# Kernel optimization log

Measured on AMD Instinct MI355X. Metric: run time of the kernel, lower is better.

## Reference

```python
import jax, jax.numpy as jnp
import numpy as np

EPS = 1e-3  # mesh.epsilon boundary margin
N_GRID = 96
F_DIM = 512


def setup_inputs() -> dict:
    key = jax.random.key(0)
    n = N_GRID
    idx = np.arange(n * n).reshape(n, n)
    # triangulated grid mesh: horizontal, vertical and diagonal edges
    e_h = np.stack([idx[:, :-1].ravel(), idx[:, 1:].ravel()])
    e_v = np.stack([idx[:-1, :].ravel(), idx[1:, :].ravel()])
    e_d = np.stack([idx[:-1, :-1].ravel(), idx[1:, 1:].ravel()])
    edges = np.concatenate([e_h, e_v, e_d], axis=1).astype(np.int32)  # [2, E]
    ys, xs = np.meshgrid(np.linspace(0.0, 1.0, n), np.linspace(0.0, 1.0, n), indexing="ij")
    vs = np.stack([xs.ravel(), ys.ravel()], axis=1).astype(np.float32)  # [V, 2]
    image = jax.random.normal(key, (n * n, F_DIM), dtype=jnp.float32)  # [V, F]
    return {"image": image, "edges": jnp.asarray(edges), "vs": jnp.asarray(vs)}


def _decimate(edges, order, adj0, boundary_v, out_target):
    """Sequential greedy edge collapse; returns (final vertex mask, collapsed flag per sorted slot).
    All carries are int/bool so this loop carries no gradient."""
    V = adj0.shape[0]
    E = order.shape[0]

    def cond(state):
        adj, mask, count, ptr, collapsed = state
        return (count > out_target) & (ptr < E)

    def body(state):
        adj, mask, count, ptr, collapsed = state
        eid = order[ptr]
        v0 = edges[0, eid]
        v1 = edges[1, eid]
        alive = mask[v0] & mask[v1]
        # neighbor sets (row | column of directed adjacency), as in is_valid
        n0 = adj[:, v0] | adj[v0, :]
        n1 = adj[:, v1] | adj[v1, :]
        shared2 = jnp.sum(n0 & n1) == 2
        do = alive & (~(boundary_v[v0] | boundary_v[v1])) & shared2

        def merge(op):
            adj, mask, count, collapsed = op
            adj = adj.at[v0, :].set(adj[v0, :] | adj[v1, :])
            adj = adj.at[:, v0].set(adj[:, v0] | adj[:, v1])
            adj = adj.at[v1, :].set(False)
            adj = adj.at[:, v1].set(False)
            adj = adj.at[v0, v0].set(False)
            mask = mask.at[v1].set(False)
            collapsed = collapsed.at[ptr].set(True)
            return adj, mask, count - 1, collapsed

        adj, mask, count, collapsed = jax.lax.cond(
            do, merge, lambda op: op, (adj, mask, count, collapsed))
        return adj, mask, count, ptr + 1, collapsed

    init = (adj0, jnp.ones((V,), dtype=bool), jnp.int32(V), jnp.int32(0),
            jnp.zeros((E,), dtype=bool))
    _, mask, _, _, collapsed = jax.lax.while_loop(cond, body, init)
    return mask, collapsed


def reference(image, edges, vs):
    V, F = image.shape
    e0, e1 = edges[0], edges[1]
    # priority = squared magnitude of concat(image[e0], image[e1]) per edge
    sq = jnp.sum(image * image, axis=1)  # [V]
    prio = sq[e0] + sq[e1]               # [E]
    # static heap pop order == stable ascending sort (ties broken by edge id)
    order = jnp.argsort(prio)
    adj0 = jnp.zeros((V, V), dtype=bool).at[e0, e1].set(True)
    b = ((vs[:, 0] < EPS) | (vs[:, 0] > 1.0 - EPS) |
         (vs[:, 1] < EPS) | (vs[:, 1] > 1.0 - EPS))
    mask, collapsed = _decimate(edges, order, adj0, b, V // 2)

    # replay collapses on features (merge_vertex -> average endpoint features)
    def step(feat, inp):
        eid, flag = inp
        v0 = edges[0, eid]
        v1 = edges[1, eid]
        feat = feat.at[v0].set(jnp.where(flag, 0.5 * (feat[v0] + feat[v1]), feat[v0]))
        return feat, None

    feat, _ = jax.lax.scan(step, image, (order, collapsed))
    return feat * mask[:, None].astype(feat.dtype)
```

## Files before the change

### kernel.cpp

```cpp
#include <hip/hip_runtime.h>
#include <stdint.h>

#define F_DIM 512
#define CAP   64
#define MAXV  9216
#define GP    4

typedef unsigned long long u64;

__global__ void k_sq(const float* __restrict__ img, double* __restrict__ sqd, int V) {
  int v = blockIdx.x;
  if (v >= V) return;
  const float* row = img + (size_t)v * F_DIM;
  double s = 0.0;
  for (int f = threadIdx.x; f < F_DIM; f += 64) {
    double x = (double)row[f];
    s += x * x;
  }
  for (int off = 32; off > 0; off >>= 1) s += __shfl_down(s, off);
  if (threadIdx.x == 0) sqd[v] = s;
}

__global__ void k_prep(const float* __restrict__ vs, const int* __restrict__ edges,
                       int V, int E, int* __restrict__ deg, unsigned char* __restrict__ elig) {
  int i = blockIdx.x * blockDim.x + threadIdx.x;
  if (i < V) deg[i] = 0;
  if (i < E) {
    int a = edges[i], b = edges[E + i];
    float ax = vs[2 * a], ay = vs[2 * a + 1];
    float bx = vs[2 * b], by = vs[2 * b + 1];
    const float eps = 1e-3f;
    const float hi = 1.0f - 1e-3f;
    bool ba = (ax < eps) || (ax > hi) || (ay < eps) || (ay > hi);
    bool bb = (bx < eps) || (bx > hi) || (by < eps) || (by > hi);
    elig[i] = (!ba && !bb) ? 1 : 0;
  }
}

__global__ void k_lists(const int* __restrict__ edges, int E,
                        int* __restrict__ deg, unsigned short* __restrict__ nbr) {
  int e = blockIdx.x * blockDim.x + threadIdx.x;
  if (e >= E) return;
  int a = edges[e], b = edges[E + e];
  int ia = atomicAdd(&deg[a], 1);
  nbr[a * CAP + ia] = (unsigned short)b;
  int ib = atomicAdd(&deg[b], 1);
  nbr[b * CAP + ib] = (unsigned short)a;
}

__global__ void k_keys(const double* __restrict__ sqd, const int* __restrict__ edges,
                       int E, int P, u64* __restrict__ keys) {
  int e = blockIdx.x * blockDim.x + threadIdx.x;
  if (e >= P) return;
  if (e < E) {
    double prio = sqd[edges[e]] + sqd[edges[E + e]];
    u64 bits = (u64)__double_as_longlong(prio);
    keys[e] = (bits & ~0xFFFFull) | (u64)e;
  } else {
    keys[e] = ~0ull;
  }
}

#define SCH 4096
__global__ void __launch_bounds__(1024)
k_sort(u64* __restrict__ keys, int n) {
  __shared__ u64 buf[SCH];
  int tid = threadIdx.x;
  int nt = blockDim.x;
  int ch = n < SCH ? n : SCH;
  for (int chunk = 0; chunk < n; chunk += ch) {
    for (int i = tid; i < ch; i += nt) buf[i] = keys[chunk + i];
    __syncthreads();
    for (int k = 2; k <= ch; k <<= 1) {
      for (int j = k >> 1; j > 0; j >>= 1) {
        for (int li = tid; li < ch; li += nt) {
          int lj = li ^ j;
          if (lj > li) {
            u64 x = buf[li], y = buf[lj];
            bool up = (((chunk + li) & k) == 0);
            if (up ? (x > y) : (x < y)) { buf[li] = y; buf[lj] = x; }
          }
        }
        __syncthreads();
      }
    }
    for (int i = tid; i < ch; i += nt) keys[chunk + i] = buf[i];
    __syncthreads();
  }
  for (int k = (ch << 1); k <= n; k <<= 1) {
    for (int j = k >> 1; j >= ch; j >>= 1) {
      for (int i = tid; i < n; i += nt) {
        int ixj = i ^ j;
        if (ixj > i) {
          u64 x = keys[i], y = keys[ixj];
          bool up = ((i & k) == 0);
          if (up ? (x > y) : (x < y)) { keys[i] = y; keys[ixj] = x; }
        }
      }
      __syncthreads();
    }
    for (int chunk = 0; chunk < n; chunk += ch) {
      for (int i = tid; i < ch; i += nt) buf[i] = keys[chunk + i];
      __syncthreads();
      for (int j = ch >> 1; j > 0; j >>= 1) {
        for (int li = tid; li < ch; li += nt) {
          int lj = li ^ j;
          if (lj > li) {
            u64 x = buf[li], y = buf[lj];
            bool up = (((chunk + li) & k) == 0);
            if (up ? (x > y) : (x < y)) { buf[li] = y; buf[lj] = x; }
          }
        }
        __syncthreads();
      }
      for (int i = tid; i < ch; i += nt) keys[chunk + i] = buf[i];
      __syncthreads();
    }
  }
}

__global__ void k_reorder(const u64* __restrict__ keys, const int* __restrict__ edges,
                          const unsigned char* __restrict__ elig, int E,
                          unsigned* __restrict__ packed) {
  int t = blockIdx.x * blockDim.x + threadIdx.x;
  if (t >= E) return;
  int eid = (int)(keys[t] & 0xFFFFull);
  unsigned v0 = (unsigned)edges[eid];
  unsigned v1 = (unsigned)edges[E + eid];
  unsigned el = (unsigned)elig[eid];
  packed[t] = v0 | (v1 << 14) | (el << 28);
}

__device__ __forceinline__ int findroot(unsigned* rs, int x) {
  while (true) {
    unsigned w = rs[x];
    int p = (int)(w & 0xFFFFu);
    if (p == x) return x;
    int q = (int)(rs[p] & 0xFFFFu);
    if (q == p) return p;
    rs[x] = (w & 0xFFFF0000u) | (unsigned)q;
    x = q;
  }
}

__global__ void __launch_bounds__(64, 1)
k_decimate(int E, int V, int target, const unsigned* __restrict__ packed,
           const int* __restrict__ deg_g, unsigned short* __restrict__ nbr,
           int2* __restrict__ events, int* __restrict__ nev_out) {
  __shared__ unsigned rs[MAXV];
  __shared__ unsigned short mkA0[MAXV], mkB0[MAXV];
  __shared__ unsigned short mkA1[MAXV], mkB1[MAXV];
  const int lane = threadIdx.x;
  const int lane_h = lane & 31;
  if (V > MAXV) return;
  for (int v = lane; v < V; v += 64) {
    rs[v] = (unsigned)v | ((unsigned)deg_g[v] << 16);
    mkA0[v] = 0; mkB0[v] = 0; mkA1[v] = 0; mkB1[v] = 0;
  }
  __syncthreads();

  int count = V, nev = 0;
  unsigned ctr = 0;
  bool stop = false, dirty = false;
  const u64 lanebit = 1ull << lane;
  const u64 below = lanebit - 1;

  auto bumpCtr = [&]() {
    ++ctr;
    if ((ctr & 1023u) == 0u) {
      for (int v = lane; v < MAXV; v += 64) { mkA0[v] = 0; mkB0[v] = 0; mkA1[v] = 0; mkB1[v] = 0; }
      asm volatile("s_waitcnt lgkmcnt(0)" ::: "memory");
      __builtin_amdgcn_sched_barrier(0);
      ++ctr;
    }
  };

  auto solo = [&](int cv0, int cv1) -> bool {
    unsigned w0 = rs[cv0], w1 = rs[cv1];
    if ((w0 & 0xFFFFu) != (unsigned)cv0 || (w1 & 0xFFFFu) != (unsigned)cv1) return false;
    int L0 = (int)(w0 >> 16), L1 = (int)(w1 >> 16);
    if (dirty) {
      asm volatile("s_waitcnt vmcnt(0)" ::: "memory");
      __builtin_amdgcn_sched_barrier(0);
      dirty = false;
    }
    unsigned rawA = (lane < L0) ? (unsigned)nbr[cv0 * CAP + lane] : 0u;
    unsigned rawB = (lane < L1) ? (unsigned)nbr[cv1 * CAP + lane] : 0u;
    int rA = 0x7FFF, rB = 0x7FFF;
    if (lane < L0) rA = findroot(rs, (int)rawA);
    if (lane < L1) rB = findroot(rs, (int)rawB);
    bumpCtr();
    unsigned tag = ctr & 1023u;
    unsigned short enc = (unsigned short)((tag << 6) | (unsigned)lane);
    bool wA = (lane < L0) && (rA != cv0);
    bool wB = (lane < L1) && (rB != cv1);
    if (wA) mkA0[rA] = enc;
    if (wB) mkB0[rB] = enc;
    asm volatile("s_waitcnt lgkmcnt(0)" ::: "memory");
    __builtin_amdgcn_sched_barrier(0);
    bool canonA = wA && (mkA0[rA] == enc);
    bool canonB = wB && (mkB0[rB] == enc);
    bool sh = canonA && ((mkB0[rA] >> 6) == tag);
    if (__popcll(__ballot(sh)) != 2) return false;
    if (L0 + L1 <= CAP) {
      if (lane < L1) nbr[cv0 * CAP + L0 + lane] = (unsigned short)rB;
      if (lane == 0) rs[cv0] = (unsigned)cv0 | ((unsigned)(L0 + L1) << 16);
    } else {
      bool pa = canonA && (rA != cv1);
      bool pb = canonB && (rB != cv0) && ((mkA0[rB] >> 6) != tag);
      u64 ma = __ballot(pa);
      u64 mb = __ballot(pb);
      int na = __popcll(ma);
      int tot = na + __popcll(mb);
      if (tot > CAP) tot = CAP;
      if (pa) nbr[cv0 * CAP + __popcll(ma & below)] = (unsigned short)rA;
      if (pb) {
        int pos = na + __popcll(mb & below);
        if (pos < CAP) nbr[cv0 * CAP + pos] = (unsigned short)rB;
      }
      if (lane == 0) rs[cv0] = (unsigned)cv0 | ((unsigned)tot << 16);
    }
    if (lane == 0) {
      rs[cv1] = (unsigned)cv0;
      events[nev] = make_int2(cv0, cv1);
    }
    asm volatile("s_waitcnt lgkmcnt(0)" ::: "memory");
    __builtin_amdgcn_sched_barrier(0);
    return true;
  };

  for (int base = 0; base < E && !stop; base += 64) {
    int t = base + lane;
    unsigned pk = (t < E) ? packed[t] : 0u;
    int mv0 = (int)(pk & 0x3FFFu);
    int mv1 = (int)((pk >> 14) & 0x3FFFu);
    bool cand = (t < E) && ((pk >> 28) & 1u) &&
                (rs[mv0] & 0xFFFFu) == (unsigned)mv0 &&
                (rs[mv1] & 0xFFFFu) == (unsigned)mv1;
    u64 cm = __ballot(cand);

    while (cm != 0 && !stop) {
      int c0A[GP], c1A[GP], c0B[GP], c1B[GP];
      unsigned ga[GP], gb[GP];
#pragma unroll
      for (int p = 0; p < GP; ++p) {
        int idA = -1, idB = -1;
        if (cm) { idA = __builtin_ctzll(cm); cm &= cm - 1; }
        if (cm) { idB = __builtin_ctzll(cm); cm &= cm - 1; }
        if (idA >= 0) {
          unsigned pkc = __builtin_amdgcn_readlane(pk, idA);
          c0A[p] = (int)(pkc & 0x3FFFu); c1A[p] = (int)((pkc >> 14) & 0x3FFFu);
        } else { c0A[p] = -1; c1A[p] = -1; }
        if (idB >= 0) {
          unsigned pkc = __builtin_amdgcn_readlane(pk, idB);
          c0B[p] = (int)(pkc & 0x3FFFu); c1B[p] = (int)((pkc >> 14) & 0x3FFFu);
        } else { c0B[p] = -1; c1B[p] = -1; }
      }
      if (dirty) {
        asm volatile("s_waitcnt vmcnt(0)" ::: "memory");
        __builtin_amdgcn_sched_barrier(0);
        dirty = false;
      }
#pragma unroll
      for (int p = 0; p < GP; ++p) {
        int cv0h = (lane < 32) ? c0A[p] : c0B[p];
        int cv1h = (lane < 32) ? c1A[p] : c1B[p];
        if (cv0h >= 0) {
          ga[p] = (unsigned)nbr[cv0h * CAP + lane_h];
          gb[p] = (unsigned)nbr[cv1h * CAP + lane_h];
        } else { ga[p] = 0; gb[p] = 0; }
      }
      int app[2 * GP];
#pragma unroll
      for (int j = 0; j < 2 * GP; ++j) app[j] = -1;

#pragma unroll
      for (int p = 0; p < GP; ++p) {
        if (c0A[p] < 0 || stop) continue;
        bool stale = false;
#pragma unroll
        for (int j = 0; j < 2 * GP; ++j) {
          if (j < 2 * p && app[j] >= 0) {
            stale = stale || app[j] == c0A[p] || app[j] == c1A[p] ||
                             app[j] == c0B[p] || app[j] == c1B[p];
          }
        }
        if (stale) {
          asm volatile("s_waitcnt vmcnt(0)" ::: "memory");
          __builtin_amdgcn_sched_barrier(0);
          dirty = false;
          int cv0h = (lane < 32) ? c0A[p] : c0B[p];
          int cv1h = (lane < 32) ? c1A[p] : c1B[p];
          if (cv0h >= 0) {
            ga[p] = (unsigned)nbr[cv0h * CAP + lane_h];
            gb[p] = (unsigned)nbr[cv1h * CAP + lane_h];
          }
        }
        int cv0 = (lane < 32) ? c0A[p] : c0B[p];
        int cv1 = (lane < 32) ? c1A[p] : c1B[p];
        bool halfAct = cv0 >= 0;
        unsigned w0 = 0, w1 = 0;
        if (halfAct) { w0 = rs[cv0]; w1 = rs[cv1]; }
        bool alive = halfAct && (w0 & 0xFFFFu) == (unsigned)cv0 &&
                                (w1 & 0xFFFFu) == (unsigned)cv1;
        int L0 = alive ? (int)(w0 >> 16) : 0;
        int L1 = alive ? (int)(w1 >> 16) : 0;
        bool paired = alive && L0 <= 32 && L1 <= 32;
        bool soloH = alive && !paired;
        u64 aliveBal = __ballot(alive);
        u64 soloBal = __ballot(soloH);
        bumpCtr();
        unsigned tag = ctr & 1023u;
        int rA = 0x7FFF, rB = 0x7FFF;
        if (paired && lane_h < L0) rA = findroot(rs, (int)(ga[p] & 0xFFFFu));
        if (paired && lane_h < L1) rB = findroot(rs, (int)(gb[p] & 0xFFFFu));
        unsigned short* mA = (lane < 32) ? mkA0 : mkA1;
        unsigned short* mB = (lane < 32) ? mkB0 : mkB1;
        unsigned short enc = (unsigned short)((tag << 6) | (unsigned)lane);
        bool wA = paired && lane_h < L0 && rA != cv0;
        bool wB = paired && lane_h < L1 && rB != cv1;
        if (wA) mA[rA] = enc;
        if (wB) mB[rB] = enc;
        asm volatile("s_waitcnt lgkmcnt(0)" ::: "memory");
        __builtin_amdgcn_sched_barrier(0);
        bool sh = wA && (mA[rA] == enc) && ((mB[rA] >> 6) == tag);
        u64 shBal = __ballot(sh);
        int cntA = __popcll(shBal & 0xFFFFFFFFull);
        int cntB = __popcll(shBal >> 32);
        bool aliveA = (aliveBal & 1ull) != 0;
        bool aliveB = ((aliveBal >> 32) & 1ull) != 0;
        bool soloA = (soloBal & 1ull) != 0;
        bool soloB = ((soloBal >> 32) & 1ull) != 0;
        int L0A = __builtin_amdgcn_readlane(L0, 0);
        int L1A = __builtin_amdgcn_readlane(L1, 0);
        int L0B = __builtin_amdgcn_readlane(L0, 32);
        int L1B = __builtin_amdgcn_readlane(L1, 32);
        bool committedA = false;
        if (aliveA) {
          if (soloA) {
            committedA = solo(c0A[p], c1A[p]);
          } else if (cntA == 2) {
            if (lane < 32 && lane_h < L1A)
              nbr[c0A[p] * CAP + L0A + lane_h] = (unsigned short)rB;
            if (lane == 0) {
              rs[c0A[p]] = (unsigned)c0A[p] | ((unsigned)(L0A + L1A) << 16);
              rs[c1A[p]] = (unsigned)c0A[p];
              events[nev] = make_int2(c0A[p], c1A[p]);
            }
            asm volatile("s_waitcnt lgkmcnt(0)" ::: "memory");
            __builtin_amdgcn_sched_barrier(0);
            committedA = true;
          }
          if (committedA) {
            app[2 * p] = c0A[p];
            nev++; count--; dirty = true;
            if (count <= target) stop = true;
          }
        }
        if (!stop && c0B[p] >= 0 && aliveB) {
          bool deadB = false, soloNeedB = soloB;
          if (committedA) {
            int c1a = c1A[p], c0a = c0A[p];
            if (c0B[p] == c1a || c1B[p] == c1a) deadB = true;
            else {
              u64 hb = __ballot((rA == c1a) || (rB == c1a));
              if (c0B[p] == c0a || c1B[p] == c0a || (hb >> 32) != 0ull) soloNeedB = true;
            }
          }
          if (!deadB) {
            bool commitB = false;
            if (soloNeedB) {
              commitB = solo(c0B[p], c1B[p]);
            } else if (cntB == 2) {
              if (lane >= 32 && lane_h < L1B)
                nbr[c0B[p] * CAP + L0B + lane_h] = (unsigned short)rB;
              if (lane == 0) {
                rs[c0B[p]] = (unsigned)c0B[p] | ((unsigned)(L0B + L1B) << 16);
                rs[c1B[p]] = (unsigned)c0B[p];
                events[nev] = make_int2(c0B[p], c1B[p]);
              }
              asm volatile("s_waitcnt lgkmcnt(0)" ::: "memory");
              __builtin_amdgcn_sched_barrier(0);
              commitB = true;
            }
            if (commitB) {
              app[2 * p + 1] = c0B[p];
              nev++; count--; dirty = true;
              if (count <= target) stop = true;
            }
          }
        }
      }
    }
  }
  if (lane == 0) nev_out[0] = nev;
}

__global__ void __launch_bounds__(256)
k_weights(const int2* __restrict__ events, const int* __restrict__ nev_p,
          int V, int* __restrict__ own, float* __restrict__ wgt) {
  __shared__ int O[MAXV];
  __shared__ unsigned short H[MAXV];
  __shared__ int2 evb[256];
  int tid = threadIdx.x;
  if (V > MAXV) return;
  for (int v = tid; v < V; v += blockDim.x) { O[v] = v; H[v] = 0; }
  int n = nev_p[0];
  __syncthreads();
  int nb = (n + 255) >> 8;
  for (int b = nb - 1; b >= 0; --b) {
    int bbase = b << 8;
    int cnt = n - bbase; if (cnt > 256) cnt = 256;
    if (tid < cnt) evb[tid] = events[bbase + tid];
    __syncthreads();
    if (tid == 0) {
      for (int k = cnt - 1; k >= 0; --k) {
        int2 ev = evb[k];
        int h = (int)H[ev.x] + 1;
        H[ev.x] = (unsigned short)h;
        H[ev.y] = (unsigned short)h;
        O[ev.y] = O[ev.x];
      }
    }
    __syncthreads();
  }
  for (int v = tid; v < V; v += blockDim.x) {
    own[v] = O[v];
    wgt[v] = ldexpf(1.0f, -(int)H[v]);
  }
}

__global__ void k_zero(float4* __restrict__ out, int n4) {
  int i = blockIdx.x * blockDim.x + threadIdx.x;
  if (i < n4) out[i] = make_float4(0.f, 0.f, 0.f, 0.f);
}

__global__ void k_scatter(const float* __restrict__ img, const int* __restrict__ own,
                          const float* __restrict__ wgt, float* __restrict__ out, int V) {
  int v = blockIdx.x;
  if (v >= V) return;
  float w = wgt[v];
  int o = own[v];
  const float* src = img + (size_t)v * F_DIM;
  float* dst = out + (size_t)o * F_DIM;
  if (w == 1.0f) {
    for (int f = threadIdx.x; f < F_DIM; f += blockDim.x) dst[f] = src[f];
  } else {
    for (int f = threadIdx.x; f < F_DIM; f += blockDim.x) atomicAdd(&dst[f], w * src[f]);
  }
}

extern "C" void kernel_launch(void* const* d_in, const int* in_sizes, int n_in,
                              void* d_out, int out_size, void* d_ws, size_t ws_size,
                              hipStream_t stream) {
  const float* img  = (const float*)d_in[0];
  const int* edges  = (const int*)d_in[1];
  const float* vs   = (const float*)d_in[2];
  int V = in_sizes[2] / 2;
  int E = in_sizes[1] / 2;
  int P = 1; while (P < E) P <<= 1;

  char* wsp = (char*)d_ws;
  size_t off = 0;
  auto alloc = [&](size_t bytes) -> void* {
    void* p = (void*)(wsp + off);
    off = (off + bytes + 255) & ~(size_t)255;
    return p;
  };
  double* sqd          = (double*)alloc((size_t)V * 8);
  u64* keys            = (u64*)alloc((size_t)P * 8);
  int* deg             = (int*)alloc((size_t)V * 4);
  unsigned short* nbr  = (unsigned short*)alloc((size_t)V * CAP * 2 + 256);
  unsigned char* elig  = (unsigned char*)alloc((size_t)E);
  unsigned* packed     = (unsigned*)alloc((size_t)E * 4);
  int2* events         = (int2*)alloc((size_t)(V / 2 + 64) * 8);
  int* nev             = (int*)alloc(256);
  int* own             = (int*)alloc((size_t)V * 4);
  float* wgt           = (float*)alloc((size_t)V * 4);

  hipLaunchKernelGGL(k_sq, dim3(V), dim3(64), 0, stream, img, sqd, V);
  int mx = V > E ? V : E;
  hipLaunchKernelGGL(k_prep, dim3((mx + 255) / 256), dim3(256), 0, stream, vs, edges, V, E, deg, elig);
  hipLaunchKernelGGL(k_lists, dim3((E + 255) / 256), dim3(256), 0, stream, edges, E, deg, nbr);
  hipLaunchKernelGGL(k_keys, dim3((P + 255) / 256), dim3(256), 0, stream, sqd, edges, E, P, keys);
  hipLaunchKernelGGL(k_sort, dim3(1), dim3(1024), 0, stream, keys, P);
  hipLaunchKernelGGL(k_reorder, dim3((E + 255) / 256), dim3(256), 0, stream, keys, edges, elig, E, packed);
  hipLaunchKernelGGL(k_decimate, dim3(1), dim3(64), 0, stream,
                     E, V, V / 2, packed, deg, nbr, events, nev);
  hipLaunchKernelGGL(k_weights, dim3(1), dim3(256), 0, stream, events, nev, V, own, wgt);
  int n4 = (V * F_DIM) / 4;
  hipLaunchKernelGGL(k_zero, dim3((n4 + 255) / 256), dim3(256), 0, stream, (float4*)d_out, n4);
  hipLaunchKernelGGL(k_scatter, dim3(V), dim3(256), 0, stream, img, own, wgt, (float*)d_out, V);
}
```

Baseline: 4.904 ms.

## Parallelize owner resolution in k_weights with pointer jumping and batch height updates

Replaces the serial reverse replay of collapse events with a parallel parent array: each collapsed vertex points at its survivor, and 14 rounds of pointer jumping across 1024 threads resolve the final owner. The remaining serial height computation runs on one thread over events staged in shared memory as 16-bit values, processing 8 events per batch with register-level dependency checks so shared-memory loads can overlap. The aim is to cut the serial latency of this single-block kernel. It adds a fixed jump-round count that assumes chains no deeper than 2^14, and caps the event count at NEVMAX.

```diff
diff --git a/kernel.cpp b/kernel.cpp
--- a/kernel.cpp
+++ b/kernel.cpp
@@ -5,6 +5,7 @@
 #define CAP   64
 #define MAXV  9216
 #define GP    4
+#define NEVMAX 4672
 
 typedef unsigned long long u64;
 
@@ -396,36 +397,64 @@
   if (lane == 0) nev_out[0] = nev;
 }
 
-__global__ void __launch_bounds__(256)
+__global__ void __launch_bounds__(1024)
 k_weights(const int2* __restrict__ events, const int* __restrict__ nev_p,
           int V, int* __restrict__ own, float* __restrict__ wgt) {
-  __shared__ int O[MAXV];
+  __shared__ unsigned short evx[NEVMAX], evy[NEVMAX];
+  __shared__ unsigned short par[MAXV];
   __shared__ unsigned short H[MAXV];
-  __shared__ int2 evb[256];
   int tid = threadIdx.x;
   if (V > MAXV) return;
-  for (int v = tid; v < V; v += blockDim.x) { O[v] = v; H[v] = 0; }
   int n = nev_p[0];
+  if (n > NEVMAX) n = NEVMAX;
+  for (int v = tid; v < V; v += 1024) { par[v] = (unsigned short)v; H[v] = 0; }
   __syncthreads();
-  int nb = (n + 255) >> 8;
-  for (int b = nb - 1; b >= 0; --b) {
-    int bbase = b << 8;
-    int cnt = n - bbase; if (cnt > 256) cnt = 256;
-    if (tid < cnt) evb[tid] = events[bbase + tid];
+  for (int k = tid; k < n; k += 1024) {
+    int2 ev = events[k];
+    evx[k] = (unsigned short)ev.x;
+    evy[k] = (unsigned short)ev.y;
+    par[ev.y] = (unsigned short)ev.x;
+  }
+  __syncthreads();
+  for (int r = 0; r < 14; ++r) {
+    for (int v = tid; v < V; v += 1024) {
+      int p = par[v];
+      int pp = par[p];
+      if (pp != p) par[v] = (unsigned short)pp;
+    }
     __syncthreads();
-    if (tid == 0) {
-      for (int k = cnt - 1; k >= 0; --k) {
-        int2 ev = evb[k];
-        int h = (int)H[ev.x] + 1;
-        H[ev.x] = (unsigned short)h;
-        H[ev.y] = (unsigned short)h;
-        O[ev.y] = O[ev.x];
-      }
-    }
-    __syncthreads();
-  }
-  for (int v = tid; v < V; v += blockDim.x) {
-    own[v] = O[v];
+  }
+  if (tid == 0) {
+    int kb0 = ((n + 7) >> 3) << 3;
+    for (int kb = kb0 - 8; kb >= 0; kb -= 8) {
+      int xs[8], ys[8], hx[8], hr[8];
+#pragma unroll
+      for (int j = 0; j < 8; ++j) {
+        int idx = kb + j;
+        if (idx < n) { xs[j] = (int)evx[idx]; ys[j] = (int)evy[idx]; }
+        else { xs[j] = -1; ys[j] = -1; }
+      }
+#pragma unroll
+      for (int j = 0; j < 8; ++j) hx[j] = (xs[j] >= 0) ? (int)H[xs[j]] : 0;
+#pragma unroll
+      for (int j = 7; j >= 0; --j) {
+        hr[j] = 0;
+        if (xs[j] < 0) continue;
+        int base = hx[j];
+#pragma unroll
+        for (int i = 0; i < 8; ++i) {
+          if (i > j && xs[i] >= 0 && (xs[j] == xs[i] || xs[j] == ys[i])) { base = hr[i]; break; }
+        }
+        int h = base + 1;
+        hr[j] = h;
+        H[xs[j]] = (unsigned short)h;
+        H[ys[j]] = (unsigned short)h;
+      }
+    }
+  }
+  __syncthreads();
+  for (int v = tid; v < V; v += 1024) {
+    own[v] = (int)par[v];
     wgt[v] = ldexpf(1.0f, -(int)H[v]);
   }
 }
@@ -487,7 +516,7 @@
   hipLaunchKernelGGL(k_reorder, dim3((E + 255) / 256), dim3(256), 0, stream, keys, edges, elig, E, packed);
   hipLaunchKernelGGL(k_decimate, dim3(1), dim3(64), 0, stream,
                      E, V, V / 2, packed, deg, nbr, events, nev);
-  hipLaunchKernelGGL(k_weights, dim3(1), dim3(256), 0, stream, events, nev, V, own, wgt);
+  hipLaunchKernelGGL(k_weights, dim3(1), dim3(1024), 0, stream, events, nev, V, own, wgt);
   int n4 = (V * F_DIM) / 4;
   hipLaunchKernelGGL(k_zero, dim3((n4 + 255) / 256), dim3(256), 0, stream, (float4*)d_out, n4);
   hipLaunchKernelGGL(k_scatter, dim3(V), dim3(256), 0, stream, img, own, wgt, (float*)d_out, V);
```

After: 5.557 ms. 13.3% more time.

## Split single-block bitonic sort into multi-block chunk sorts and global merge steps

Applied to the files above, without the earlier changes.

Replaces the one-workgroup bitonic sort with a multi-block version. Each 4096-key chunk is sorted in shared memory by its own block, cross-chunk compare-exchange stages run as separate grid-wide kernel launches, and in-chunk merge tails run per block. This is meant to use the whole GPU rather than one compute unit for the sort, at the cost of several extra kernel launches. The decimation kernel remains single-block and probably dominates the runtime.

```diff
diff --git a/kernel.cpp b/kernel.cpp
--- a/kernel.cpp
+++ b/kernel.cpp
@@ -5,6 +5,7 @@
 #define CAP   64
 #define MAXV  9216
 #define GP    4
+#define SCH   4096
 
 typedef unsigned long long u64;
 
@@ -61,62 +62,58 @@
   }
 }
 
-#define SCH 4096
 __global__ void __launch_bounds__(1024)
-k_sort(u64* __restrict__ keys, int n) {
+k_sortA(u64* __restrict__ keys, int ch) {
   __shared__ u64 buf[SCH];
+  int chunk = blockIdx.x * ch;
   int tid = threadIdx.x;
-  int nt = blockDim.x;
-  int ch = n < SCH ? n : SCH;
-  for (int chunk = 0; chunk < n; chunk += ch) {
-    for (int i = tid; i < ch; i += nt) buf[i] = keys[chunk + i];
+  for (int i = tid; i < ch; i += 1024) buf[i] = keys[chunk + i];
+  __syncthreads();
+  for (int k = 2; k <= ch; k <<= 1) {
+    for (int j = k >> 1; j > 0; j >>= 1) {
+      for (int li = tid; li < ch; li += 1024) {
+        int lj = li ^ j;
+        if (lj > li) {
+          u64 x = buf[li], y = buf[lj];
+          bool up = (((chunk + li) & k) == 0);
+          if (up ? (x > y) : (x < y)) { buf[li] = y; buf[lj] = x; }
+        }
+      }
+      __syncthreads();
+    }
+  }
+  for (int i = tid; i < ch; i += 1024) keys[chunk + i] = buf[i];
+}
+
+__global__ void k_gstep(u64* __restrict__ keys, int j, int k) {
+  int t = blockIdx.x * blockDim.x + threadIdx.x;
+  int lo = t & (j - 1);
+  int i = ((t - lo) << 1) + lo;
+  int p = i + j;
+  u64 x = keys[i], y = keys[p];
+  bool up = ((i & k) == 0);
+  if (up ? (x > y) : (x < y)) { keys[i] = y; keys[p] = x; }
+}
+
+__global__ void __launch_bounds__(1024)
+k_sortB(u64* __restrict__ keys, int ch, int k) {
+  __shared__ u64 buf[SCH];
+  int chunk = blockIdx.x * ch;
+  int tid = threadIdx.x;
+  for (int i = tid; i < ch; i += 1024) buf[i] = keys[chunk + i];
+  __syncthreads();
+  bool up = ((chunk & k) == 0);
+  for (int j = ch >> 1; j > 0; j >>= 1) {
+    for (int li = tid; li < ch; li += 1024) {
+      int lj = li ^ j;
+      if (lj > li) {
+        u64 x = buf[li], y = buf[lj];
+        if (up ? (x > y) : (x < y)) { buf[li] = y; buf[lj] = x; }
+      }
+    }
     __syncthreads();
-    for (int k = 2; k <= ch; k <<= 1) {
-      for (int j = k >> 1; j > 0; j >>= 1) {
-        for (int li = tid; li < ch; li += nt) {
-          int lj = li ^ j;
-          if (lj > li) {
-            u64 x = buf[li], y = buf[lj];
-            bool up = (((chunk + li) & k) == 0);
-            if (up ? (x > y) : (x < y)) { buf[li] = y; buf[lj] = x; }
-          }
-        }
-        __syncthreads();
-      }
-    }
-    for (int i = tid; i < ch; i += nt) keys[chunk + i] = buf[i];
-    __syncthreads();
-  }
-  for (int k = (ch << 1); k <= n; k <<= 1) {
-    for (int j = k >> 1; j >= ch; j >>= 1) {
-      for (int i = tid; i < n; i += nt) {
-        int ixj = i ^ j;
-        if (ixj > i) {
-          u64 x = keys[i], y = keys[ixj];
-          bool up = ((i & k) == 0);
-          if (up ? (x > y) : (x < y)) { keys[i] = y; keys[ixj] = x; }
-        }
-      }
-      __syncthreads();
-    }
-    for (int chunk = 0; chunk < n; chunk += ch) {
-      for (int i = tid; i < ch; i += nt) buf[i] = keys[chunk + i];
-      __syncthreads();
-      for (int j = ch >> 1; j > 0; j >>= 1) {
-        for (int li = tid; li < ch; li += nt) {
-          int lj = li ^ j;
-          if (lj > li) {
-            u64 x = buf[li], y = buf[lj];
-            bool up = (((chunk + li) & k) == 0);
-            if (up ? (x > y) : (x < y)) { buf[li] = y; buf[lj] = x; }
-          }
-        }
-        __syncthreads();
-      }
-      for (int i = tid; i < ch; i += nt) keys[chunk + i] = buf[i];
-      __syncthreads();
-    }
-  }
+  }
+  for (int i = tid; i < ch; i += 1024) keys[chunk + i] = buf[i];
 }
 
 __global__ void k_reorder(const u64* __restrict__ keys, const int* __restrict__ edges,
@@ -483,7 +480,16 @@
   hipLaunchKernelGGL(k_prep, dim3((mx + 255) / 256), dim3(256), 0, stream, vs, edges, V, E, deg, elig);
   hipLaunchKernelGGL(k_lists, dim3((E + 255) / 256), dim3(256), 0, stream, edges, E, deg, nbr);
   hipLaunchKernelGGL(k_keys, dim3((P + 255) / 256), dim3(256), 0, stream, sqd, edges, E, P, keys);
-  hipLaunchKernelGGL(k_sort, dim3(1), dim3(1024), 0, stream, keys, P);
+
+  int ch = P < SCH ? P : SCH;
+  hipLaunchKernelGGL(k_sortA, dim3(P / ch), dim3(1024), 0, stream, keys, ch);
+  for (int k = ch << 1; k <= P; k <<= 1) {
+    for (int j = k >> 1; j >= ch; j >>= 1) {
+      hipLaunchKernelGGL(k_gstep, dim3(P / 512), dim3(256), 0, stream, keys, j, k);
+    }
+    hipLaunchKernelGGL(k_sortB, dim3(P / ch), dim3(1024), 0, stream, keys, ch, k);
+  }
+
   hipLaunchKernelGGL(k_reorder, dim3((E + 255) / 256), dim3(256), 0, stream, keys, edges, elig, E, packed);
   hipLaunchKernelGGL(k_decimate, dim3(1), dim3(64), 0, stream,
                      E, V, V / 2, packed, deg, nbr, events, nev);
```

Result: faster. 4.257 ms, median of 2 (-13.2%).
